# Kernel optimization log

Measured on AMD Instinct MI355X. Metric: run time of the kernel, lower is better.

Reference implementation:

```python
import jax, jax.numpy as jnp
import numpy as np

D_MODEL = 1024
NUM_HEADS = 16
NEG_INF = jnp.float32(-(2.0 ** 32) + 1.0)  # matches TF's -2**32+1 padding value


def setup_inputs() -> dict:
    key = jax.random.key(0)
    ks = jax.random.split(key, 10)
    B, S, D = 4, 1024, D_MODEL
    s = 1.0 / np.sqrt(D)
    return {
        "q": jax.random.normal(ks[0], (B, S, D), jnp.float32),
        "k": jax.random.normal(ks[1], (B, S, D), jnp.float32),
        "v": jax.random.normal(ks[2], (B, S, D), jnp.float32),
        "mask": jax.random.randint(ks[3], (NUM_HEADS * B, 1, S), 0, 2, jnp.int32),
        "Wq": jax.random.normal(ks[4], (D, D), jnp.float32) * s,
        "bq": jnp.zeros((D,), jnp.float32),
        "Wk": jax.random.normal(ks[5], (D, D), jnp.float32) * s,
        "bk": jnp.zeros((D,), jnp.float32),
        "Wv": jax.random.normal(ks[6], (D, D), jnp.float32) * s,
        "bv": jnp.zeros((D,), jnp.float32),
    }


def _split_heads(x, h):
    # TF: concat(split(x, h, axis=2), axis=0) -> head index leading on batch dim
    B, S, D = x.shape
    dh = D // h
    return x.reshape(B, S, h, dh).transpose(2, 0, 1, 3).reshape(h * B, S, dh)


def _merge_heads(x, h):
    hB, S, dh = x.shape
    B = hB // h
    return x.reshape(h, B, S, dh).transpose(1, 2, 0, 3).reshape(B, S, h * dh)


def reference(q, k, v, mask, Wq, bq, Wk, bk, Wv, bv):
    h = NUM_HEADS
    qp = q @ Wq + bq
    kp = k @ Wk + bk
    vp = v @ Wv + bv
    qh = _split_heads(qp, h)  # [h*B, S, dh]
    kh = _split_heads(kp, h)
    vh = _split_heads(vp, h)
    dh = kh.shape[-1]
    logits = jnp.einsum('bqd,bkd->bqk', qh, kh) / jnp.sqrt(jnp.float32(dh))
    logits = jnp.where(mask == 0, NEG_INF, logits)  # padding mask, broadcast [h*B,1,S]
    S = qh.shape[1]
    causal = jnp.tril(jnp.ones((S, S), jnp.bool_))
    logits = jnp.where(causal[None], logits, NEG_INF)
    attn = jax.nn.softmax(logits, axis=-1)
    out = jnp.einsum('bqk,bkd->bqd', attn, vh)
    return _merge_heads(out, h)  # [B, S, d_model]
```

## Files before the change

### kernel.cpp

```cpp
#include <hip/hip_runtime.h>
#include <stdint.h>

#define DEV __device__ __forceinline__

typedef __attribute__((ext_vector_type(4))) float f32x4;
typedef __attribute__((ext_vector_type(8))) __bf16 bf16x8;
typedef __attribute__((ext_vector_type(8))) unsigned short ushort8;
typedef __attribute__((ext_vector_type(4))) unsigned short u16x4;
typedef __attribute__((ext_vector_type(4))) int i32x4;
typedef __attribute__((ext_vector_type(2))) unsigned int u32x2;

DEV unsigned short f2bf(float f) {
    union { float f; unsigned int u; } v; v.f = f;
    unsigned int r = v.u + 0x7FFFu + ((v.u >> 16) & 1u);
    return (unsigned short)(r >> 16);
}
DEV float bf2f(unsigned short u) {
    union { unsigned int u; float f; } v; v.u = ((unsigned int)u) << 16;
    return v.f;
}
DEV unsigned int cvt_pk_bf16(float lo, float hi) {
    unsigned int r;
    asm("v_cvt_pk_bf16_f32 %0, %1, %2" : "=v"(r) : "v"(lo), "v"(hi));
    return r;
}
DEV int swz(int o) { return o ^ ((o >> 3) & 0x70); }

DEV void gload_lds16(const void* gptr, void* lptr) {
    __builtin_amdgcn_global_load_lds(
        (const __attribute__((address_space(1))) unsigned int*)gptr,
        (__attribute__((address_space(3))) unsigned int*)lptr, 16, 0, 0);
}

__global__ void k_prep(const float* __restrict__ q, const float* __restrict__ k,
                       const float* __restrict__ v, const float* __restrict__ Wq,
                       const float* __restrict__ Wk, const float* __restrict__ Wv,
                       unsigned short* __restrict__ qb, unsigned short* __restrict__ kb,
                       unsigned short* __restrict__ vb, unsigned short* __restrict__ wt) {
    __shared__ float tile[64 * 65];
    const int z = blockIdx.z;
    const int bx = blockIdx.x;
    const int t = threadIdx.x;
    if (bx < 2048) {
        const float* src = z == 0 ? q : (z == 1 ? k : v);
        unsigned short* dst = z == 0 ? qb : (z == 1 ? kb : vb);
        const size_t idx = ((size_t)bx * 256 + t) * 8;
        f32x4 a = *(const f32x4*)(src + idx);
        f32x4 b = *(const f32x4*)(src + idx + 4);
        ushort8 o;
        o[0] = f2bf(a[0]); o[1] = f2bf(a[1]); o[2] = f2bf(a[2]); o[3] = f2bf(a[3]);
        o[4] = f2bf(b[0]); o[5] = f2bf(b[1]); o[6] = f2bf(b[2]); o[7] = f2bf(b[3]);
        *(ushort8*)(dst + idx) = o;
    } else {
        const int b = bx - 2048;
        const float* W = z == 0 ? Wq : (z == 1 ? Wk : Wv);
        unsigned short* dst = wt + (size_t)z * 1048576;
        const int k0 = (b & 15) * 64, n0 = (b >> 4) * 64;
#pragma unroll
        for (int i = 0; i < 4; i++) {
            const int idx = i * 256 + t;
            const int row = idx >> 4, c4 = (idx & 15) * 4;
            f32x4 val = *(const f32x4*)(W + (size_t)(k0 + row) * 1024 + n0 + c4);
#pragma unroll
            for (int j = 0; j < 4; j++) tile[row * 65 + c4 + j] = val[j];
        }
        __syncthreads();
#pragma unroll
        for (int i = 0; i < 2; i++) {
            const int idx = i * 256 + t;
            const int nrow = idx >> 3, c8 = (idx & 7) * 8;
            ushort8 o;
#pragma unroll
            for (int j = 0; j < 8; j++) o[j] = f2bf(tile[(c8 + j) * 65 + nrow]);
            *(ushort8*)(dst + (size_t)(n0 + nrow) * 1024 + k0 + c8) = o;
        }
    }
}

__global__ __launch_bounds__(256) void k_proj(
    const unsigned short* __restrict__ qb, const unsigned short* __restrict__ kb,
    const unsigned short* __restrict__ vb, const unsigned short* __restrict__ wt,
    const float* __restrict__ bq, const float* __restrict__ bk, const float* __restrict__ bv,
    unsigned short* __restrict__ qh, unsigned short* __restrict__ kh,
    unsigned short* __restrict__ vt) {
    const int z = blockIdx.z;
    const unsigned short* A  = z == 0 ? qb : (z == 1 ? kb : vb);
    const unsigned short* Bt = wt + (size_t)z * 1048576;
    const float* bias = z == 0 ? bq : (z == 1 ? bk : bv);
    const float scale = z == 0 ? 0.18033688011112042f : 1.0f;

    __shared__ unsigned short sA[2][128 * 64];
    __shared__ unsigned short sB[2][128 * 64];

    const int tid = threadIdx.x;
    const int w = tid >> 6, lane = tid & 63;
    const int c = lane & 15, gq = lane >> 4;
    const int wrow = w >> 1, wcol = w & 1;
    const int orig = blockIdx.x;
    const int wg = (orig & 7) * 32 + (orig >> 3);
    const int n0 = (wg & 7) * 128;
    const int m0 = (wg >> 3) * 128;
    const int lr = lane >> 3;
    const int lcs = ((lane & 7) ^ (lane >> 3)) * 8;

    f32x4 acc[4][4] = {};

    auto stageAB = [&](int kt, int buf) {
        const int kb0 = kt * 64;
#pragma unroll
        for (int i = 0; i < 4; i++) {
            const int rbase = w * 32 + i * 8;
            gload_lds16(A  + (size_t)(m0 + rbase + lr) * 1024 + kb0 + lcs,
                        (char*)sA[buf] + rbase * 128);
            gload_lds16(Bt + (size_t)(n0 + rbase + lr) * 1024 + kb0 + lcs,
                        (char*)sB[buf] + rbase * 128);
        }
    };

    stageAB(0, 0);
    stageAB(1, 1);

    for (int kt = 0; kt < 16; kt++) {
        const int cur = kt & 1;
        if (kt < 15) asm volatile("s_waitcnt vmcnt(8)" ::: "memory");
        else         asm volatile("s_waitcnt vmcnt(0)" ::: "memory");
        __builtin_amdgcn_s_barrier();
        __builtin_amdgcn_sched_barrier(0);
#pragma unroll
        for (int kk = 0; kk < 2; kk++) {
            bf16x8 af[4], bfr[4];
#pragma unroll
            for (int i = 0; i < 4; i++) {
                af[i]  = *(const bf16x8*)((char*)sA[cur] +
                          swz((wrow * 64 + i * 16 + c) * 128 + kk * 64 + gq * 16));
                bfr[i] = *(const bf16x8*)((char*)sB[cur] +
                          swz((wcol * 64 + i * 16 + c) * 128 + kk * 64 + gq * 16));
            }
#pragma unroll
            for (int mi = 0; mi < 4; mi++)
#pragma unroll
                for (int ni = 0; ni < 4; ni++)
                    acc[mi][ni] = __builtin_amdgcn_mfma_f32_16x16x32_bf16(
                        af[mi], bfr[ni], acc[mi][ni], 0, 0, 0);
        }
        __builtin_amdgcn_sched_barrier(0);
        __builtin_amdgcn_s_barrier();
        if (kt + 2 < 16) stageAB(kt + 2, cur);
    }

    float bvals[4];
#pragma unroll
    for (int ni = 0; ni < 4; ni++) bvals[ni] = bias[n0 + wcol * 64 + ni * 16 + c];

    if (z < 2) {
        unsigned short* outp = z == 0 ? qh : kh;
#pragma unroll
        for (int mi = 0; mi < 4; mi++)
#pragma unroll
            for (int ni = 0; ni < 4; ni++) {
                const int n = n0 + wcol * 64 + ni * 16 + c;
                const int head = n >> 6, d = n & 63;
#pragma unroll
                for (int r = 0; r < 4; r++) {
                    const int m = m0 + wrow * 64 + mi * 16 + gq * 4 + r;
                    const int bb = m >> 10, s = m & 1023;
                    const float val = (acc[mi][ni][r] + bvals[ni]) * scale;
                    outp[(size_t)((head << 2) + bb) * 65536 + (size_t)s * 64 + d] = f2bf(val);
                }
            }
    } else {
#pragma unroll
        for (int mi = 0; mi < 4; mi++)
#pragma unroll
            for (int ni = 0; ni < 4; ni++) {
                const int n = n0 + wcol * 64 + ni * 16 + c;
                const int head = n >> 6, d = n & 63;
                const int mbase = m0 + wrow * 64 + mi * 16 + gq * 4;
                const int bb = mbase >> 10, sloc = mbase & 1023;
                u16x4 o;
#pragma unroll
                for (int r = 0; r < 4; r++) o[r] = f2bf(acc[mi][ni][r] + bvals[ni]);
                *(u16x4*)(vt + (size_t)((head << 2) + bb) * 65536 +
                          (size_t)d * 1024 + sloc) = o;
            }
    }
}

__global__ void k_vmean(const unsigned short* __restrict__ vt, float* __restrict__ vmean) {
    __shared__ float red[256];
    const int hb = blockIdx.x, t = threadIdx.x;
    const int d = t >> 2, part = t & 3;
    const unsigned short* p = vt + (size_t)hb * 65536 + (size_t)d * 1024 + part * 256;
    float sum = 0.f;
#pragma unroll 4
    for (int i = 0; i < 32; i++) {
        ushort8 v8 = *(const ushort8*)(p + i * 8);
#pragma unroll
        for (int j = 0; j < 8; j++) sum += bf2f(v8[j]);
    }
    red[t] = sum;
    __syncthreads();
    if (part == 0)
        vmean[hb * 64 + d] = (red[t] + red[t + 1] + red[t + 2] + red[t + 3]) * (1.0f / 1024.0f);
}

__global__ __launch_bounds__(256) void k_attn(
    const unsigned short* __restrict__ qh, const unsigned short* __restrict__ kh,
    const unsigned short* __restrict__ vt, const int* __restrict__ mask,
    const float* __restrict__ vmean, float* __restrict__ out,
    char* __restrict__ part) {
    __shared__ unsigned short sK[2][64 * 64];
    __shared__ unsigned short sV[2][64 * 64];
    __shared__ unsigned short sP[4 * 16 * 64];

    const int idx = blockIdx.x, hb = blockIdx.y;
    int qt, ch, nch;
    if (idx < 4)       { qt = idx;                 ch = 0;             nch = 1; }
    else if (idx < 12) { qt = 4 + ((idx - 4) >> 1);  ch = (idx - 4) & 1;  nch = 2; }
    else if (idx < 24) { int r = idx - 12; qt = 8 + r / 3; ch = r % 3;   nch = 3; }
    else               { qt = 12 + ((idx - 24) >> 2); ch = (idx - 24) & 3; nch = 4; }
    const int t0 = ch * 4;
    const int t1 = min(t0 + 4, qt + 1);

    const int tid = threadIdx.x;
    const int w = tid >> 6, lane = tid & 63;
    const int c = lane & 15, g = lane >> 4, g4 = g * 4;
    const int q0 = qt * 64 + w * 16;
    const int qg = q0 + c;
    const size_t hboff = (size_t)hb * 65536;
    const int* mp = mask + hb * 1024;
    unsigned short* pw = sP + w * 1024;

    bf16x8 aq[2];
#pragma unroll
    for (int kk = 0; kk < 2; kk++)
        aq[kk] = *(const bf16x8*)(qh + hboff + (size_t)qg * 64 + kk * 32 + g * 8);

    f32x4 oacc[4] = {};
    float lsum = 0.f, mrow = -1e30f;

    const int srow = tid >> 3, sch = tid & 7;
    const int ssc = (sch ^ (srow & 7)) * 8;

    auto stage = [&](int t, int buf) {
        const int kv0 = t * 64;
#pragma unroll
        for (int i = 0; i < 2; i++) {
            const int row = i * 32 + srow;
            gload_lds16(kh + hboff + (size_t)(kv0 + row) * 64 + ssc,
                        (char*)sK[buf] + row * 128 + sch * 16);
        }
#pragma unroll
        for (int i = 0; i < 2; i++) {
            const int row = i * 32 + srow;
            gload_lds16(vt + hboff + (size_t)row * 1024 + kv0 + ssc,
                        (char*)sV[buf] + row * 128 + sch * 16);
        }
    };

    stage(t0, 0);
    for (int t = t0; t < t1; t++) {
        const int cur = (t - t0) & 1;
        if (t + 1 < t1) {
            stage(t + 1, cur ^ 1);
            asm volatile("s_waitcnt vmcnt(4)" ::: "memory");
        } else {
            asm volatile("s_waitcnt vmcnt(0)" ::: "memory");
        }
        __builtin_amdgcn_s_barrier();
        __builtin_amdgcn_sched_barrier(0);

        const int kv0 = t * 64;
        const bool diag = (t == qt);
        const unsigned short* sKc = sK[cur];
        const unsigned short* sVc = sV[cur];

        f32x4 sacc[4] = {};
#pragma unroll
        for (int ns = 0; ns < 4; ns++)
#pragma unroll
            for (int kk = 0; kk < 2; kk++) {
                const bf16x8 bk = *(const bf16x8*)((char*)sKc +
                                    swz((ns * 16 + c) * 128 + kk * 64 + g * 16));
                sacc[ns] = __builtin_amdgcn_mfma_f32_16x16x32_bf16(bk, aq[kk], sacc[ns], 0, 0, 0);
            }

        float sv[4][4];
        float mx = -1e30f;
#pragma unroll
        for (int ns = 0; ns < 4; ns++) {
            const i32x4 mm = *(const i32x4*)(mp + kv0 + ns * 16 + g4);
#pragma unroll
            for (int r = 0; r < 4; r++) {
                float s = (mm[r] != 0) ? sacc[ns][r] : -1e30f;
                if (diag) s = (kv0 + ns * 16 + g4 + r <= qg) ? s : -1e30f;
                sv[ns][r] = s;
                mx = fmaxf(mx, s);
            }
        }
        mx = fmaxf(mx, __shfl_xor(mx, 16, 64));
        mx = fmaxf(mx, __shfl_xor(mx, 32, 64));
        const float mnew = fmaxf(mrow, mx);
        const float alpha = exp2f(mrow - mnew);
        mrow = mnew;

        float rs = 0.f;
        u32x2 pk[4];
#pragma unroll
        for (int ns = 0; ns < 4; ns++) {
            const float e0 = exp2f(sv[ns][0] - mnew);
            const float e1 = exp2f(sv[ns][1] - mnew);
            const float e2 = exp2f(sv[ns][2] - mnew);
            const float e3 = exp2f(sv[ns][3] - mnew);
            rs += (e0 + e1) + (e2 + e3);
            pk[ns][0] = cvt_pk_bf16(e0, e1);
            pk[ns][1] = cvt_pk_bf16(e2, e3);
        }
        rs += __shfl_xor(rs, 16, 64);
        rs += __shfl_xor(rs, 32, 64);
        lsum = lsum * alpha + rs;

#pragma unroll
        for (int ns = 0; ns < 4; ns++)
            *(u32x2*)((char*)pw + swz(c * 128 + (ns * 16 + g4) * 2)) = pk[ns];

        float av[4];
#pragma unroll
        for (int r = 0; r < 4; r++) av[r] = __shfl(alpha, g4 + r, 16);
#pragma unroll
        for (int nd = 0; nd < 4; nd++)
#pragma unroll
            for (int r = 0; r < 4; r++) oacc[nd][r] *= av[r];

        asm volatile("s_waitcnt lgkmcnt(0)" ::: "memory");
#pragma unroll
        for (int ks = 0; ks < 2; ks++) {
            const bf16x8 ap = *(const bf16x8*)((char*)pw + swz(c * 128 + ks * 64 + g * 16));
#pragma unroll
            for (int nd = 0; nd < 4; nd++) {
                const bf16x8 bvv = *(const bf16x8*)((char*)sVc +
                                     swz((nd * 16 + c) * 128 + ks * 64 + g * 16));
                oacc[nd] = __builtin_amdgcn_mfma_f32_16x16x32_bf16(ap, bvv, oacc[nd], 0, 0, 0);
            }
        }
        __builtin_amdgcn_sched_barrier(0);
        __builtin_amdgcn_s_barrier();
        __builtin_amdgcn_sched_barrier(0);
    }

    if (nch == 1) {
        const int bidx = hb & 3, head = hb >> 2;
        float lf[4], mf[4];
#pragma unroll
        for (int r = 0; r < 4; r++) {
            lf[r] = __shfl(lsum, g4 + r, 16);
            mf[r] = __shfl(mrow, g4 + r, 16);
        }
#pragma unroll
        for (int nd = 0; nd < 4; nd++)
#pragma unroll
            for (int r = 0; r < 4; r++) {
                const int s = q0 + g4 + r;
                const int dcol = nd * 16 + c;
                const float val = (mf[r] < -5e29f) ? vmean[hb * 64 + dcol]
                                                   : oacc[nd][r] / lf[r];
                out[(size_t)bidx * 1048576 + (size_t)s * 1024 + head * 64 + dcol] = val;
            }
    } else {
        char* sp = part + ((size_t)hb * 36 + (idx - 4)) * 8704;
        unsigned short* op = (unsigned short*)sp;
#pragma unroll
        for (int nd = 0; nd < 4; nd++)
#pragma unroll
            for (int r = 0; r < 4; r++)
                op[(w * 16 + g4 + r) * 64 + nd * 16 + c] = f2bf(oacc[nd][r]);
        if (g == 0) {
            float* mo = (float*)(sp + 8192);
            float* lo = (float*)(sp + 8448);
            mo[w * 16 + c] = mrow;
            lo[w * 16 + c] = lsum;
        }
    }
}

__global__ __launch_bounds__(256) void k_combine(
    const char* __restrict__ part, const float* __restrict__ vmean,
    float* __restrict__ out) {
    const int qt = 4 + blockIdx.x, hb = blockIdx.y;
    int nch, base;
    if (qt < 8)       { nch = 2; base = (qt - 4) * 2; }
    else if (qt < 12) { nch = 3; base = 8 + (qt - 8) * 3; }
    else              { nch = 4; base = 20 + (qt - 12) * 4; }
    const int t = threadIdx.x;
    const int row = t >> 2, d0 = (t & 3) * 16;
    const char* sp0 = part + ((size_t)hb * 36 + base) * 8704;

    float mi[4], li[4];
    float m = -1e30f;
#pragma unroll
    for (int i = 0; i < 4; i++)
        if (i < nch) {
            const char* sp = sp0 + (size_t)i * 8704;
            mi[i] = ((const float*)(sp + 8192))[row];
            li[i] = ((const float*)(sp + 8448))[row];
            m = fmaxf(m, mi[i]);
        }
    float L = 0.f;
    float o[16];
#pragma unroll
    for (int j = 0; j < 16; j++) o[j] = 0.f;
#pragma unroll
    for (int i = 0; i < 4; i++)
        if (i < nch) {
            const float wgt = exp2f(mi[i] - m);
            L += wgt * li[i];
            const unsigned short* op =
                (const unsigned short*)(sp0 + (size_t)i * 8704) + row * 64 + d0;
            ushort8 a = *(const ushort8*)op;
            ushort8 b = *(const ushort8*)(op + 8);
#pragma unroll
            for (int j = 0; j < 8; j++) {
                o[j]     += wgt * bf2f(a[j]);
                o[8 + j] += wgt * bf2f(b[j]);
            }
        }
    const int bidx = hb & 3, head = hb >> 2;
    float* dst = out + (size_t)bidx * 1048576 + (size_t)(qt * 64 + row) * 1024 + head * 64 + d0;
    if (m > -5e29f) {
        const float inv = 1.0f / L;
#pragma unroll
        for (int j = 0; j < 16; j++) dst[j] = o[j] * inv;
    } else {
#pragma unroll
        for (int j = 0; j < 16; j++) dst[j] = vmean[hb * 64 + d0 + j];
    }
}

extern "C" void kernel_launch(void* const* d_in, const int* in_sizes, int n_in,
                              void* d_out, int out_size, void* d_ws, size_t ws_size,
                              hipStream_t stream) {
    const float* q  = (const float*)d_in[0];
    const float* k  = (const float*)d_in[1];
    const float* v  = (const float*)d_in[2];
    const int* mask = (const int*)d_in[3];
    const float* Wq = (const float*)d_in[4];
    const float* bq = (const float*)d_in[5];
    const float* Wk = (const float*)d_in[6];
    const float* bk = (const float*)d_in[7];
    const float* Wv = (const float*)d_in[8];
    const float* bv = (const float*)d_in[9];
    float* out = (float*)d_out;

    unsigned short* qb = (unsigned short*)d_ws;
    unsigned short* kb = qb + 4194304;
    unsigned short* vb = kb + 4194304;
    unsigned short* wt = vb + 4194304;
    unsigned short* qh = wt + 3 * 1048576;
    unsigned short* kh = qh + 4194304;
    unsigned short* vh = kh + 4194304;
    unsigned short* vt = vh + 4194304;
    float* vmean = (float*)(vt + 4194304);
    char* part = (char*)qb;

    k_prep<<<dim3(2304, 1, 3), 256, 0, stream>>>(q, k, v, Wq, Wk, Wv, qb, kb, vb, wt);
    k_proj<<<dim3(256, 1, 3), 256, 0, stream>>>(qb, kb, vb, wt, bq, bk, bv, qh, kh, vt);
    k_vmean<<<64, 256, 0, stream>>>(vt, vmean);
    k_attn<<<dim3(40, 64), 256, 0, stream>>>(qh, kh, vt, mask, vmean, out, part);
    k_combine<<<dim3(12, 64), 256, 0, stream>>>(part, vmean, out);
}
```

Before: 207.8 us.

## Fuse fp32-to-bf16 activation conversion into projection GEMM A-tile staging

Removes the separate conversion pass that wrote bf16 copies of q, k and v, and has the projection kernel load fp32 activations into registers, convert them with packed bf16 instructions, and write them into LDS. The prep kernel now only transposes and converts the weights. This cuts a full read-and-write round trip of the activations through global memory. In exchange the GEMM reads twice as many A bytes, uses more registers for the staging buffers, and gets a more manual pipeline with extra waits and barriers.

```diff
diff --git a/kernel.cpp b/kernel.cpp
--- a/kernel.cpp
+++ b/kernel.cpp
@@ -9,6 +9,7 @@
 typedef __attribute__((ext_vector_type(4))) unsigned short u16x4;
 typedef __attribute__((ext_vector_type(4))) int i32x4;
 typedef __attribute__((ext_vector_type(2))) unsigned int u32x2;
+typedef __attribute__((ext_vector_type(4))) unsigned int u32x4;
 
 DEV unsigned short f2bf(float f) {
     union { float f; unsigned int u; } v; v.f = f;
@@ -32,59 +33,43 @@
         (__attribute__((address_space(3))) unsigned int*)lptr, 16, 0, 0);
 }
 
-__global__ void k_prep(const float* __restrict__ q, const float* __restrict__ k,
-                       const float* __restrict__ v, const float* __restrict__ Wq,
-                       const float* __restrict__ Wk, const float* __restrict__ Wv,
-                       unsigned short* __restrict__ qb, unsigned short* __restrict__ kb,
-                       unsigned short* __restrict__ vb, unsigned short* __restrict__ wt) {
+__global__ void k_prep(const float* __restrict__ Wq, const float* __restrict__ Wk,
+                       const float* __restrict__ Wv, unsigned short* __restrict__ wt) {
     __shared__ float tile[64 * 65];
     const int z = blockIdx.z;
-    const int bx = blockIdx.x;
+    const float* W = z == 0 ? Wq : (z == 1 ? Wk : Wv);
+    unsigned short* dst = wt + (size_t)z * 1048576;
+    const int b = blockIdx.x;
+    const int k0 = (b & 15) * 64, n0 = (b >> 4) * 64;
     const int t = threadIdx.x;
-    if (bx < 2048) {
-        const float* src = z == 0 ? q : (z == 1 ? k : v);
-        unsigned short* dst = z == 0 ? qb : (z == 1 ? kb : vb);
-        const size_t idx = ((size_t)bx * 256 + t) * 8;
-        f32x4 a = *(const f32x4*)(src + idx);
-        f32x4 b = *(const f32x4*)(src + idx + 4);
+#pragma unroll
+    for (int i = 0; i < 4; i++) {
+        const int idx = i * 256 + t;
+        const int row = idx >> 4, c4 = (idx & 15) * 4;
+        f32x4 val = *(const f32x4*)(W + (size_t)(k0 + row) * 1024 + n0 + c4);
+#pragma unroll
+        for (int j = 0; j < 4; j++) tile[row * 65 + c4 + j] = val[j];
+    }
+    __syncthreads();
+#pragma unroll
+    for (int i = 0; i < 2; i++) {
+        const int idx = i * 256 + t;
+        const int nrow = idx >> 3, c8 = (idx & 7) * 8;
         ushort8 o;
-        o[0] = f2bf(a[0]); o[1] = f2bf(a[1]); o[2] = f2bf(a[2]); o[3] = f2bf(a[3]);
-        o[4] = f2bf(b[0]); o[5] = f2bf(b[1]); o[6] = f2bf(b[2]); o[7] = f2bf(b[3]);
-        *(ushort8*)(dst + idx) = o;
-    } else {
-        const int b = bx - 2048;
-        const float* W = z == 0 ? Wq : (z == 1 ? Wk : Wv);
-        unsigned short* dst = wt + (size_t)z * 1048576;
-        const int k0 = (b & 15) * 64, n0 = (b >> 4) * 64;
-#pragma unroll
-        for (int i = 0; i < 4; i++) {
-            const int idx = i * 256 + t;
-            const int row = idx >> 4, c4 = (idx & 15) * 4;
-            f32x4 val = *(const f32x4*)(W + (size_t)(k0 + row) * 1024 + n0 + c4);
-#pragma unroll
-            for (int j = 0; j < 4; j++) tile[row * 65 + c4 + j] = val[j];
-        }
-        __syncthreads();
-#pragma unroll
-        for (int i = 0; i < 2; i++) {
-            const int idx = i * 256 + t;
-            const int nrow = idx >> 3, c8 = (idx & 7) * 8;
-            ushort8 o;
-#pragma unroll
-            for (int j = 0; j < 8; j++) o[j] = f2bf(tile[(c8 + j) * 65 + nrow]);
-            *(ushort8*)(dst + (size_t)(n0 + nrow) * 1024 + k0 + c8) = o;
-        }
+#pragma unroll
+        for (int j = 0; j < 8; j++) o[j] = f2bf(tile[(c8 + j) * 65 + nrow]);
+        *(ushort8*)(dst + (size_t)(n0 + nrow) * 1024 + k0 + c8) = o;
     }
 }
 
 __global__ __launch_bounds__(256) void k_proj(
-    const unsigned short* __restrict__ qb, const unsigned short* __restrict__ kb,
-    const unsigned short* __restrict__ vb, const unsigned short* __restrict__ wt,
+    const float* __restrict__ qf, const float* __restrict__ kf,
+    const float* __restrict__ vf, const unsigned short* __restrict__ wt,
     const float* __restrict__ bq, const float* __restrict__ bk, const float* __restrict__ bv,
     unsigned short* __restrict__ qh, unsigned short* __restrict__ kh,
     unsigned short* __restrict__ vt) {
     const int z = blockIdx.z;
-    const unsigned short* A  = z == 0 ? qb : (z == 1 ? kb : vb);
+    const float* A32 = z == 0 ? qf : (z == 1 ? kf : vf);
     const unsigned short* Bt = wt + (size_t)z * 1048576;
     const float* bias = z == 0 ? bq : (z == 1 ? bk : bv);
     const float scale = z == 0 ? 0.18033688011112042f : 1.0f;
@@ -104,28 +89,38 @@
     const int lcs = ((lane & 7) ^ (lane >> 3)) * 8;
 
     f32x4 acc[4][4] = {};
-
-    auto stageAB = [&](int kt, int buf) {
+    f32x4 rA0[8], rA1[8];
+
+    auto issueA = [&](int kt, f32x4* ra) {
+        const int kb0 = kt * 64;
+#pragma unroll
+        for (int i = 0; i < 4; i++) {
+            const float* src = A32 + (size_t)(m0 + w * 32 + i * 8 + lr) * 1024 + kb0 + lcs;
+            ra[2 * i]     = *(const f32x4*)src;
+            ra[2 * i + 1] = *(const f32x4*)(src + 4);
+        }
+    };
+    auto writeA = [&](const f32x4* ra, int buf) {
+#pragma unroll
+        for (int i = 0; i < 4; i++) {
+            u32x4 o;
+            o[0] = cvt_pk_bf16(ra[2 * i][0],     ra[2 * i][1]);
+            o[1] = cvt_pk_bf16(ra[2 * i][2],     ra[2 * i][3]);
+            o[2] = cvt_pk_bf16(ra[2 * i + 1][0], ra[2 * i + 1][1]);
+            o[3] = cvt_pk_bf16(ra[2 * i + 1][2], ra[2 * i + 1][3]);
+            *(u32x4*)((char*)sA[buf] + (w * 32 + i * 8) * 128 + lane * 16) = o;
+        }
+    };
+    auto stageB = [&](int kt, int buf) {
         const int kb0 = kt * 64;
 #pragma unroll
         for (int i = 0; i < 4; i++) {
             const int rbase = w * 32 + i * 8;
-            gload_lds16(A  + (size_t)(m0 + rbase + lr) * 1024 + kb0 + lcs,
-                        (char*)sA[buf] + rbase * 128);
             gload_lds16(Bt + (size_t)(n0 + rbase + lr) * 1024 + kb0 + lcs,
                         (char*)sB[buf] + rbase * 128);
         }
     };
-
-    stageAB(0, 0);
-    stageAB(1, 1);
-
-    for (int kt = 0; kt < 16; kt++) {
-        const int cur = kt & 1;
-        if (kt < 15) asm volatile("s_waitcnt vmcnt(8)" ::: "memory");
-        else         asm volatile("s_waitcnt vmcnt(0)" ::: "memory");
-        __builtin_amdgcn_s_barrier();
-        __builtin_amdgcn_sched_barrier(0);
+    auto compute = [&](int cur) {
 #pragma unroll
         for (int kk = 0; kk < 2; kk++) {
             bf16x8 af[4], bfr[4];
@@ -143,9 +138,44 @@
                     acc[mi][ni] = __builtin_amdgcn_mfma_f32_16x16x32_bf16(
                         af[mi], bfr[ni], acc[mi][ni], 0, 0, 0);
         }
-        __builtin_amdgcn_sched_barrier(0);
-        __builtin_amdgcn_s_barrier();
-        if (kt + 2 < 16) stageAB(kt + 2, cur);
+    };
+
+    issueA(0, rA0); stageB(0, 0);
+    issueA(1, rA1); stageB(1, 1);
+    asm volatile("s_waitcnt vmcnt(12)" ::: "memory");
+    writeA(rA0, 0);
+    asm volatile("s_waitcnt lgkmcnt(0)" ::: "memory");
+    __builtin_amdgcn_s_barrier();
+
+    for (int kt2 = 0; kt2 < 16; kt2 += 2) {
+        {
+            const int kt = kt2;
+            compute(0);
+            __builtin_amdgcn_sched_barrier(0);
+            __builtin_amdgcn_s_barrier();
+            if (kt < 14) { issueA(kt + 2, rA0); stageB(kt + 2, 0); }
+            if (kt < 15) {
+                if (kt < 14) asm volatile("s_waitcnt vmcnt(12)" ::: "memory");
+                else         asm volatile("s_waitcnt vmcnt(0)" ::: "memory");
+                writeA(rA1, 1);
+                asm volatile("s_waitcnt lgkmcnt(0)" ::: "memory");
+            }
+            __builtin_amdgcn_s_barrier();
+        }
+        {
+            const int kt = kt2 + 1;
+            compute(1);
+            __builtin_amdgcn_sched_barrier(0);
+            __builtin_amdgcn_s_barrier();
+            if (kt < 14) { issueA(kt + 2, rA1); stageB(kt + 2, 1); }
+            if (kt < 15) {
+                if (kt < 14) asm volatile("s_waitcnt vmcnt(12)" ::: "memory");
+                else         asm volatile("s_waitcnt vmcnt(0)" ::: "memory");
+                writeA(rA0, 0);
+                asm volatile("s_waitcnt lgkmcnt(0)" ::: "memory");
+            }
+            __builtin_amdgcn_s_barrier();
+        }
     }
 
     float bvals[4];
@@ -452,9 +482,7 @@
     float* out = (float*)d_out;
 
     unsigned short* qb = (unsigned short*)d_ws;
-    unsigned short* kb = qb + 4194304;
-    unsigned short* vb = kb + 4194304;
-    unsigned short* wt = vb + 4194304;
+    unsigned short* wt = qb + 3 * 4194304;
     unsigned short* qh = wt + 3 * 1048576;
     unsigned short* kh = qh + 4194304;
     unsigned short* vh = kh + 4194304;
@@ -462,8 +490,8 @@
     float* vmean = (float*)(vt + 4194304);
     char* part = (char*)qb;
 
-    k_prep<<<dim3(2304, 1, 3), 256, 0, stream>>>(q, k, v, Wq, Wk, Wv, qb, kb, vb, wt);
-    k_proj<<<dim3(256, 1, 3), 256, 0, stream>>>(qb, kb, vb, wt, bq, bk, bv, qh, kh, vt);
+    k_prep<<<dim3(256, 1, 3), 256, 0, stream>>>(Wq, Wk, Wv, wt);
+    k_proj<<<dim3(256, 1, 3), 256, 0, stream>>>(q, k, v, wt, bq, bk, bv, qh, kh, vt);
     k_vmean<<<64, 256, 0, stream>>>(vt, vmean);
     k_attn<<<dim3(40, 64), 256, 0, stream>>>(qh, kh, vt, mask, vmean, out, part);
     k_combine<<<dim3(12, 64), 256, 0, stream>>>(part, vmean, out);
```

Measured after the change: 236.4 us. 1.14x slower.
